# Performance work log

Measured on AMD Instinct MI355X. Metric: run time of the kernel, lower is better.

Reference implementation:

```python
import jax, jax.numpy as jnp
import numpy as np

TAU = 1.0            # temperature (self.temperature.item())
FAST_WEIGHT_DECAY = 0.01
FAST_WEIGHT_LR = 0.01

B, IN, H = 128, 1024, 1024


def setup_inputs() -> dict:
    key = jax.random.key(0)
    k = jax.random.split(key, 6)
    scale_ih = 1.0 / np.sqrt(IN)
    scale_hh = np.sqrt(2.0 / (H + H))  # xavier_uniform-like std
    return {
        "x_t": jax.random.normal(k[0], (B, IN), jnp.float32),
        "h_prev": jax.random.normal(k[1], (B, H), jnp.float32),
        "W_ih": jax.random.normal(k[2], (H, IN), jnp.float32) * scale_ih,
        "b_ih": jnp.zeros((H,), jnp.float32),
        "W_hh_fixed": jax.random.normal(k[3], (H, H), jnp.float32) * scale_hh,
        "W_hh_virtual": jnp.zeros((H, H), jnp.float32),
        "gumbel_u": jax.random.uniform(k[4], (B, H, H), jnp.float32),
    }


def reference(x_t, h_prev, W_ih, b_ih, W_hh_fixed, W_hh_virtual, gumbel_u):
    # input contribution: Linear(input_size, hidden_size)
    input_contrib = x_t @ W_ih.T + b_ih                      # (B, H)

    # logits scaled by temperature once, then gumbel_softmax divides by tau again
    logits = (W_hh_fixed + W_hh_virtual) / TAU               # (H, H)
    eps = 1e-9
    g = -jnp.log(-jnp.log(jnp.clip(gumbel_u, eps, 1.0 - eps)))  # Gumbel(0,1), (B,H,H)
    y = jax.nn.softmax((logits[None, :, :] + g) / TAU, axis=2)  # soft sampling, (B,H,H)

    # weighted exchange: each output neuron o reduces sampled weights against h_prev
    contrib = jnp.einsum('boh,bh->bo', y, h_prev)            # (B, H)
    h_next = jnp.tanh(input_contrib + contrib)               # (B, H)

    # Hebbian fast-weight update (no_grad in original)
    hebbian = jnp.einsum('bo,bh->oh', h_next, h_prev) / B    # mean over batch, (H,H)
    W_hh_virtual_new = jax.lax.stop_gradient(
        W_hh_virtual * (1.0 - FAST_WEIGHT_DECAY) + hebbian * FAST_WEIGHT_LR
    )
    return h_next, W_hh_virtual_new
```

## Files before the change

### kernel.cpp

```cpp
#include <hip/hip_runtime.h>
#include <hip/hip_bf16.h>
#include <cstddef>

#define B_DIM  128
#define IN_DIM 1024
#define H_DIM  1024

constexpr float kDecay   = 1.0f - 0.01f;
constexpr float kLrOverB = 0.01f / 128.0f;

typedef float f32x4 __attribute__((ext_vector_type(4)));

__global__ __launch_bounds__(256) void exp_logits(
    const float* __restrict__ W_f,
    const float* __restrict__ W_v,
    float* __restrict__ E)
{
    const int i = blockIdx.x * 256 + threadIdx.x;
    const float4 a = reinterpret_cast<const float4*>(W_f)[i];
    const float4 b = reinterpret_cast<const float4*>(W_v)[i];
    float4 e;
    e.x = __expf(a.x + b.x); e.y = __expf(a.y + b.y);
    e.z = __expf(a.z + b.z); e.w = __expf(a.w + b.w);
    reinterpret_cast<float4*>(E)[i] = e;
}

__global__ __launch_bounds__(256) void input_gemm(
    const float* __restrict__ x_t,
    const float* __restrict__ W_ih,
    const float* __restrict__ b_ih,
    float* __restrict__ ic)
{
    const int o0 = blockIdx.x * 64;
    const int b0 = blockIdx.y * 16;
    const int t  = threadIdx.x;

    __shared__ float Wt[64][68];
    __shared__ float xs[64][17];

    const int tx = t & 15;
    const int ty = t >> 4;

    float acc[4] = {0.f, 0.f, 0.f, 0.f};

    for (int kc = 0; kc < IN_DIM / 64; ++kc) {
        const int k0 = kc * 64;

#pragma unroll
        for (int ii = 0; ii < 4; ++ii) {
            const int i  = t + 256 * ii;
            const int r  = i >> 4;
            const int c4 = (i & 15) * 4;
            const float4 wv = *reinterpret_cast<const float4*>(
                &W_ih[(size_t)(o0 + r) * IN_DIM + k0 + c4]);
            Wt[c4 + 0][r] = wv.x; Wt[c4 + 1][r] = wv.y;
            Wt[c4 + 2][r] = wv.z; Wt[c4 + 3][r] = wv.w;
        }
        {
            const int br = t >> 4;
            const int c4 = (t & 15) * 4;
            const float4 xv = *reinterpret_cast<const float4*>(
                &x_t[(size_t)(b0 + br) * IN_DIM + k0 + c4]);
            xs[c4 + 0][br] = xv.x; xs[c4 + 1][br] = xv.y;
            xs[c4 + 2][br] = xv.z; xs[c4 + 3][br] = xv.w;
        }
        __syncthreads();

#pragma unroll 8
        for (int k = 0; k < 64; ++k) {
            const float  xb = xs[k][ty];
            const float4 wv = *reinterpret_cast<const float4*>(&Wt[k][4 * tx]);
            acc[0] = fmaf(wv.x, xb, acc[0]);
            acc[1] = fmaf(wv.y, xb, acc[1]);
            acc[2] = fmaf(wv.z, xb, acc[2]);
            acc[3] = fmaf(wv.w, xb, acc[3]);
        }
        __syncthreads();
    }

    const int o = o0 + 4 * tx;
    const int b = b0 + ty;
    float4 r;
    r.x = acc[0] + b_ih[o + 0];
    r.y = acc[1] + b_ih[o + 1];
    r.z = acc[2] + b_ih[o + 2];
    r.w = acc[3] + b_ih[o + 3];
    *reinterpret_cast<float4*>(&ic[(size_t)b * H_DIM + o]) = r;
}

__global__ __launch_bounds__(256) void fused_rows(
    const float* __restrict__ h_prev,
    const float* __restrict__ E,
    const float* __restrict__ gu,
    const float* __restrict__ ic,
    float* __restrict__ h_next)
{
    const int b0 = blockIdx.x * 8;
    const int o0 = blockIdx.y * 16;
    const int t  = threadIdx.x;
    const int w  = t >> 6, lane = t & 63;

    __shared__ __align__(16) float hp_s[8 * H_DIM];

    {
        const float4* src = reinterpret_cast<const float4*>(h_prev) + (size_t)b0 * 256;
        float4*       dst = reinterpret_cast<float4*>(hp_s);
#pragma unroll
        for (int ii = 0; ii < 8; ++ii) dst[t + 256 * ii] = src[t + 256 * ii];
    }
    __syncthreads();

    const int orow0 = o0 + w * 4;

    float4 e[4][4];
    {
        const float4* E4 = reinterpret_cast<const float4*>(E) + (size_t)orow0 * 256;
#pragma unroll
        for (int r = 0; r < 4; ++r)
#pragma unroll
            for (int j = 0; j < 4; ++j)
                e[r][j] = E4[r * 256 + lane + 64 * j];
    }

    const float4* hp4 = reinterpret_cast<const float4*>(hp_s);

    for (int bb = 0; bb < 8; ++bb) {
        const int b = b0 + bb;
        const f32x4* g4 = reinterpret_cast<const f32x4*>(gu)
                        + ((size_t)b * H_DIM + orow0) * 256;

        f32x4 u[4][4];
#pragma unroll
        for (int r = 0; r < 4; ++r)
#pragma unroll
            for (int j = 0; j < 4; ++j)
                u[r][j] = __builtin_nontemporal_load(g4 + (r * 4 + j) * 64 + lane);

        float4 p[4];
#pragma unroll
        for (int j = 0; j < 4; ++j) p[j] = hp4[bb * 256 + lane + 64 * j];

        float s[4], d[4];
#pragma unroll
        for (int r = 0; r < 4; ++r) {
            float sum = 0.f, dot = 0.f;
#pragma unroll
            for (int j = 0; j < 4; ++j) {
                const f32x4 uu = u[r][j];
                const float4 ee = e[r][j];
                const float4 pp = p[j];
                const float q0 = __fdividef(ee.x, -__log2f(fmaxf(uu.x, 1e-9f)));
                const float q1 = __fdividef(ee.y, -__log2f(fmaxf(uu.y, 1e-9f)));
                const float q2 = __fdividef(ee.z, -__log2f(fmaxf(uu.z, 1e-9f)));
                const float q3 = __fdividef(ee.w, -__log2f(fmaxf(uu.w, 1e-9f)));
                sum += (q0 + q1) + (q2 + q3);
                dot = fmaf(q0, pp.x, dot);
                dot = fmaf(q1, pp.y, dot);
                dot = fmaf(q2, pp.z, dot);
                dot = fmaf(q3, pp.w, dot);
            }
            s[r] = sum;
            d[r] = dot;
        }

#pragma unroll
        for (int off = 32; off > 0; off >>= 1) {
#pragma unroll
            for (int r = 0; r < 4; ++r) {
                s[r] += __shfl_xor(s[r], off, 64);
                d[r] += __shfl_xor(d[r], off, 64);
            }
        }

        if (lane == 0) {
#pragma unroll
            for (int r = 0; r < 4; ++r) {
                const size_t idx = (size_t)b * H_DIM + orow0 + r;
                h_next[idx] = tanhf(ic[idx] + __fdividef(d[r], s[r]));
            }
        }
    }
}

__global__ __launch_bounds__(256) void hebbian_update(
    const float* __restrict__ h_next,
    const float* __restrict__ h_prev,
    const float* __restrict__ W_v,
    float* __restrict__ W_out)
{
    const int h0 = blockIdx.x * 64;
    const int o0 = blockIdx.y * 64;
    const int t  = threadIdx.x;

    __shared__ __align__(16) float hn_s[B_DIM][64];
    __shared__ __align__(16) float hp_s[B_DIM][64];

#pragma unroll
    for (int i = 0; i < 32; ++i) {
        const int e  = t + 256 * i;
        const int bb = e >> 6;
        const int cc = e & 63;
        hn_s[bb][cc] = h_next[(size_t)bb * H_DIM + o0 + cc];
        hp_s[bb][cc] = h_prev[(size_t)bb * H_DIM + h0 + cc];
    }
    __syncthreads();

    const int tx = t & 15;
    const int ty = t >> 4;

    float acc[4][4] = {{0.f}};

#pragma unroll 8
    for (int b = 0; b < B_DIM; ++b) {
        const float4 av = reinterpret_cast<const float4*>(hn_s[b])[ty];
        const float4 bv = reinterpret_cast<const float4*>(hp_s[b])[tx];
        const float aa[4] = {av.x, av.y, av.z, av.w};
        const float bb[4] = {bv.x, bv.y, bv.z, bv.w};
#pragma unroll
        for (int a = 0; a < 4; ++a)
#pragma unroll
            for (int c = 0; c < 4; ++c)
                acc[a][c] = fmaf(aa[a], bb[c], acc[a][c]);
    }

#pragma unroll
    for (int a = 0; a < 4; ++a) {
        const int o = o0 + 4 * ty + a;
        const size_t base = (size_t)o * H_DIM + h0 + 4 * tx;
        const float4 wv = *reinterpret_cast<const float4*>(W_v + base);
        float4 r;
        r.x = wv.x * kDecay + acc[a][0] * kLrOverB;
        r.y = wv.y * kDecay + acc[a][1] * kLrOverB;
        r.z = wv.z * kDecay + acc[a][2] * kLrOverB;
        r.w = wv.w * kDecay + acc[a][3] * kLrOverB;
        *reinterpret_cast<float4*>(W_out + base) = r;
    }
}

extern "C" void kernel_launch(void* const* d_in, const int* in_sizes, int n_in,
                              void* d_out, int out_size, void* d_ws, size_t ws_size,
                              hipStream_t stream)
{
    const float* x_t    = (const float*)d_in[0];
    const float* h_prev = (const float*)d_in[1];
    const float* W_ih   = (const float*)d_in[2];
    const float* b_ih   = (const float*)d_in[3];
    const float* W_f    = (const float*)d_in[4];
    const float* W_v    = (const float*)d_in[5];
    const float* gu     = (const float*)d_in[6];

    float* out    = (float*)d_out;
    float* h_next = out;
    float* W_out  = out + (size_t)B_DIM * H_DIM;

    float* E  = (float*)d_ws;
    float* ic = E + (size_t)H_DIM * H_DIM;

    exp_logits<<<dim3(H_DIM * H_DIM / 1024), 256, 0, stream>>>(W_f, W_v, E);

    input_gemm<<<dim3(H_DIM / 64, B_DIM / 16), 256, 0, stream>>>(
        x_t, W_ih, b_ih, ic);

    fused_rows<<<dim3(B_DIM / 8, H_DIM / 16), 256, 0, stream>>>(
        h_prev, E, gu, ic, h_next);

    hebbian_update<<<dim3(H_DIM / 64, H_DIM / 64), 256, 0, stream>>>(
        h_next, h_prev, W_v, W_out);
}
```

Baseline: 154.9 us.

## Restructure fused_rows: stage E rows in LDS, one batch per wave, double-buffer gumbel loads

```diff
diff --git a/kernel.cpp b/kernel.cpp
--- a/kernel.cpp
+++ b/kernel.cpp
@@ -88,97 +88,105 @@
     *reinterpret_cast<float4*>(&ic[(size_t)b * H_DIM + o]) = r;
 }
 
-__global__ __launch_bounds__(256) void fused_rows(
+__global__ __launch_bounds__(256, 4) void fused_rows(
     const float* __restrict__ h_prev,
     const float* __restrict__ E,
     const float* __restrict__ gu,
     const float* __restrict__ ic,
     float* __restrict__ h_next)
 {
-    const int b0 = blockIdx.x * 8;
-    const int o0 = blockIdx.y * 16;
+    const int b0 = blockIdx.x * 4;
+    const int o0 = blockIdx.y * 8;
     const int t  = threadIdx.x;
     const int w  = t >> 6, lane = t & 63;
 
-    __shared__ __align__(16) float hp_s[8 * H_DIM];
+    __shared__ __align__(16) float e_s[8 * H_DIM];
 
     {
-        const float4* src = reinterpret_cast<const float4*>(h_prev) + (size_t)b0 * 256;
-        float4*       dst = reinterpret_cast<float4*>(hp_s);
+        const float4* src = reinterpret_cast<const float4*>(E) + (size_t)o0 * 256;
+        float4*       dst = reinterpret_cast<float4*>(e_s);
 #pragma unroll
         for (int ii = 0; ii < 8; ++ii) dst[t + 256 * ii] = src[t + 256 * ii];
     }
     __syncthreads();
 
-    const int orow0 = o0 + w * 4;
-
-    float4 e[4][4];
-    {
-        const float4* E4 = reinterpret_cast<const float4*>(E) + (size_t)orow0 * 256;
-#pragma unroll
-        for (int r = 0; r < 4; ++r)
-#pragma unroll
-            for (int j = 0; j < 4; ++j)
-                e[r][j] = E4[r * 256 + lane + 64 * j];
-    }
-
-    const float4* hp4 = reinterpret_cast<const float4*>(hp_s);
-
-    for (int bb = 0; bb < 8; ++bb) {
-        const int b = b0 + bb;
-        const f32x4* g4 = reinterpret_cast<const f32x4*>(gu)
-                        + ((size_t)b * H_DIM + orow0) * 256;
-
-        f32x4 u[4][4];
-#pragma unroll
-        for (int r = 0; r < 4; ++r)
-#pragma unroll
-            for (int j = 0; j < 4; ++j)
-                u[r][j] = __builtin_nontemporal_load(g4 + (r * 4 + j) * 64 + lane);
-
-        float4 p[4];
-#pragma unroll
-        for (int j = 0; j < 4; ++j) p[j] = hp4[bb * 256 + lane + 64 * j];
-
-        float s[4], d[4];
-#pragma unroll
-        for (int r = 0; r < 4; ++r) {
-            float sum = 0.f, dot = 0.f;
-#pragma unroll
-            for (int j = 0; j < 4; ++j) {
-                const f32x4 uu = u[r][j];
-                const float4 ee = e[r][j];
-                const float4 pp = p[j];
-                const float q0 = __fdividef(ee.x, -__log2f(fmaxf(uu.x, 1e-9f)));
-                const float q1 = __fdividef(ee.y, -__log2f(fmaxf(uu.y, 1e-9f)));
-                const float q2 = __fdividef(ee.z, -__log2f(fmaxf(uu.z, 1e-9f)));
-                const float q3 = __fdividef(ee.w, -__log2f(fmaxf(uu.w, 1e-9f)));
-                sum += (q0 + q1) + (q2 + q3);
-                dot = fmaf(q0, pp.x, dot);
-                dot = fmaf(q1, pp.y, dot);
-                dot = fmaf(q2, pp.z, dot);
-                dot = fmaf(q3, pp.w, dot);
+    const int b = b0 + w;
+
+    const float4* hp4 = reinterpret_cast<const float4*>(h_prev + (size_t)b * H_DIM);
+    float4 p[4];
+#pragma unroll
+    for (int j = 0; j < 4; ++j) p[j] = hp4[lane + 64 * j];
+
+    const f32x4*  g4 = reinterpret_cast<const f32x4*>(gu)
+                     + ((size_t)b * H_DIM + o0) * 256;
+    const float4* e4 = reinterpret_cast<const float4*>(e_s);
+
+    f32x4 ua[4], ub[4];
+    float s[8], d[8];
+
+#pragma unroll
+    for (int j = 0; j < 4; ++j)
+        ua[j] = __builtin_nontemporal_load(g4 + lane + 64 * j);
+
+#pragma unroll
+    for (int oi = 0; oi < 8; ++oi) {
+        if (oi < 7) {
+            const f32x4* gn = g4 + (size_t)(oi + 1) * 256;
+            if ((oi & 1) == 0) {
+#pragma unroll
+                for (int j = 0; j < 4; ++j)
+                    ub[j] = __builtin_nontemporal_load(gn + lane + 64 * j);
+            } else {
+#pragma unroll
+                for (int j = 0; j < 4; ++j)
+                    ua[j] = __builtin_nontemporal_load(gn + lane + 64 * j);
             }
-            s[r] = sum;
-            d[r] = dot;
-        }
-
-#pragma unroll
-        for (int off = 32; off > 0; off >>= 1) {
-#pragma unroll
-            for (int r = 0; r < 4; ++r) {
-                s[r] += __shfl_xor(s[r], off, 64);
-                d[r] += __shfl_xor(d[r], off, 64);
-            }
-        }
-
-        if (lane == 0) {
-#pragma unroll
-            for (int r = 0; r < 4; ++r) {
-                const size_t idx = (size_t)b * H_DIM + orow0 + r;
-                h_next[idx] = tanhf(ic[idx] + __fdividef(d[r], s[r]));
-            }
-        }
+        }
+
+        float sum = 0.f, dot = 0.f;
+#pragma unroll
+        for (int j = 0; j < 4; ++j) {
+            const f32x4  uu = (oi & 1) ? ub[j] : ua[j];
+            const float4 ee = e4[oi * 256 + lane + 64 * j];
+            const float4 pp = p[j];
+            const float q0 = __fdividef(ee.x, -__log2f(fmaxf(uu.x, 1e-9f)));
+            const float q1 = __fdividef(ee.y, -__log2f(fmaxf(uu.y, 1e-9f)));
+            const float q2 = __fdividef(ee.z, -__log2f(fmaxf(uu.z, 1e-9f)));
+            const float q3 = __fdividef(ee.w, -__log2f(fmaxf(uu.w, 1e-9f)));
+            sum += (q0 + q1) + (q2 + q3);
+            dot = fmaf(q0, pp.x, dot);
+            dot = fmaf(q1, pp.y, dot);
+            dot = fmaf(q2, pp.z, dot);
+            dot = fmaf(q3, pp.w, dot);
+        }
+        s[oi] = sum;
+        d[oi] = dot;
+    }
+
+#pragma unroll
+    for (int off = 32; off > 0; off >>= 1) {
+#pragma unroll
+        for (int r = 0; r < 8; ++r) {
+            s[r] += __shfl_xor(s[r], off, 64);
+            d[r] += __shfl_xor(d[r], off, 64);
+        }
+    }
+
+    if (lane == 0) {
+        const size_t base = (size_t)b * H_DIM + o0;
+        const float4 i0 = *reinterpret_cast<const float4*>(ic + base);
+        const float4 i1 = *reinterpret_cast<const float4*>(ic + base + 4);
+        float4 r0, r1;
+        r0.x = tanhf(i0.x + __fdividef(d[0], s[0]));
+        r0.y = tanhf(i0.y + __fdividef(d[1], s[1]));
+        r0.z = tanhf(i0.z + __fdividef(d[2], s[2]));
+        r0.w = tanhf(i0.w + __fdividef(d[3], s[3]));
+        r1.x = tanhf(i1.x + __fdividef(d[4], s[4]));
+        r1.y = tanhf(i1.y + __fdividef(d[5], s[5]));
+        r1.z = tanhf(i1.z + __fdividef(d[6], s[6]));
+        r1.w = tanhf(i1.w + __fdividef(d[7], s[7]));
+        *reinterpret_cast<float4*>(h_next + base)     = r0;
+        *reinterpret_cast<float4*>(h_next + base + 4) = r1;
     }
 }
 
@@ -261,7 +269,7 @@
     input_gemm<<<dim3(H_DIM / 64, B_DIM / 16), 256, 0, stream>>>(
         x_t, W_ih, b_ih, ic);
 
-    fused_rows<<<dim3(B_DIM / 8, H_DIM / 16), 256, 0, stream>>>(
+    fused_rows<<<dim3(B_DIM / 4, H_DIM / 8), 256, 0, stream>>>(
         h_prev, E, gu, ic, h_next);
 
     hebbian_update<<<dim3(H_DIM / 64, H_DIM / 64), 256, 0, stream>>>(
```

Result: faster. 144.1 us (-6.9%).
